# Kernel tuning notes

Hardware: AMD Instinct MI355X
Metric: run time of the kernel (lower is better)

Reference implementation:

```python
import jax, jax.numpy as jnp
import numpy as np

B, C, H, W = 16, 384, 56, 56
NH, WS, SS = 12, 7, 3          # num_heads, window_size, shift_size
MLP = 4 * C
N = WS * WS                     # tokens per window (49)
nHW = H // WS                   # windows per side (8)
nW = nHW * nHW                  # windows per image (64)
HD = C // NH                    # head dim (32)
EPS = 1e-5


def _ln(x, g, b):
    mu = jnp.mean(x, axis=-1, keepdims=True)
    var = jnp.mean(jnp.square(x - mu), axis=-1, keepdims=True)
    return (x - mu) * jax.lax.rsqrt(var + EPS) * g + b


def _attn_mask():
    # static shifted-window mask, computed once with numpy (constants)
    img = np.zeros((H, W))
    sl = (slice(0, -WS), slice(-WS, -SS), slice(-SS, None))
    cnt = 0
    for hs in sl:
        for ws_ in sl:
            img[hs, ws_] = cnt
            cnt += 1
    mw = img.reshape(nHW, WS, nHW, WS).transpose(0, 2, 1, 3).reshape(-1, N)
    d = mw[:, None, :] - mw[:, :, None]          # (nW, N, N)
    return jnp.asarray(np.where(d != 0, -100.0, 0.0), jnp.float32)

_MASK = _attn_mask()


def setup_inputs() -> dict:
    key = jax.random.key(0)
    ks = jax.random.split(key, 6)
    rn = lambda k, s: jax.random.normal(k, s, jnp.float32) * 0.02
    return {
        "x": jax.random.normal(ks[0], (B, C, H, W), jnp.float32),
        "norm1_g": jnp.ones((C,), jnp.float32),
        "norm1_b": jnp.zeros((C,), jnp.float32),
        "qkv_w": rn(ks[1], (C, 3 * C)),
        "qkv_b": jnp.zeros((3 * C,), jnp.float32),
        "proj_w": rn(ks[2], (C, C)),
        "proj_b": jnp.zeros((C,), jnp.float32),
        "norm2_g": jnp.ones((C,), jnp.float32),
        "norm2_b": jnp.zeros((C,), jnp.float32),
        "fc1_w": rn(ks[3], (C, MLP)),
        "fc1_b": jnp.zeros((MLP,), jnp.float32),
        "fc2_w": rn(ks[4], (MLP, C)),
        "fc2_b": jnp.zeros((C,), jnp.float32),
    }


def reference(x, norm1_g, norm1_b, qkv_w, qkv_b, proj_w, proj_b,
              norm2_g, norm2_b, fc1_w, fc1_b, fc2_w, fc2_b):
    shortcut = x                                   # (B, C, H, W)
    xh = jnp.transpose(x, (0, 2, 3, 1))            # (B, H, W, C)
    xh = _ln(xh, norm1_g, norm1_b)
    # H, W divisible by WS -> padding is a no-op; shifted window path
    xs = jnp.roll(xh, (-SS, -SS), axis=(1, 2))
    # window partition -> (B*nW, N, C)
    xw = xs.reshape(B, nHW, WS, nHW, WS, C).transpose(0, 1, 3, 2, 4, 5)
    xw = xw.reshape(-1, N, C)
    # attention
    qkv = (xw @ qkv_w + qkv_b).reshape(-1, N, 3, NH, HD).transpose(2, 0, 3, 1, 4)
    q, k, v = qkv[0] * HD ** -0.5, qkv[1], qkv[2]  # (B*nW, NH, N, HD)
    attn = jnp.einsum('whnd,whmd->whnm', q, k)     # (B*nW, NH, N, N)
    attn = attn.reshape(B, nW, NH, N, N) + _MASK[None, :, None]
    attn = jax.nn.softmax(attn, axis=-1).reshape(-1, NH, N, N)
    out = jnp.einsum('whnm,whmd->whnd', attn, v)   # (B*nW, NH, N, HD)
    out = out.transpose(0, 2, 1, 3).reshape(-1, N, C)
    out = out @ proj_w + proj_b
    # window reverse -> (B, H, W, C), un-shift
    xs = out.reshape(B, nHW, nHW, WS, WS, C).transpose(0, 1, 3, 2, 4, 5)
    xs = xs.reshape(B, H, W, C)
    xh = jnp.roll(xs, (SS, SS), axis=(1, 2))
    x2 = shortcut + jnp.transpose(xh, (0, 3, 1, 2))
    # MLP residual (in BHWC)
    xh2 = jnp.transpose(x2, (0, 2, 3, 1))
    h = jax.nn.gelu(_ln(xh2, norm2_g, norm2_b) @ fc1_w + fc1_b,
                    approximate=False) @ fc2_w + fc2_b
    xh2 = xh2 + h
    return jnp.transpose(xh2, (0, 3, 1, 2))
```

## Files before the change

### kernel.cpp

```cpp
#include <hip/hip_runtime.h>
#include <hip/hip_bf16.h>
#include <math.h>
#include <stdint.h>

#define C_ 384
#define TOKENS 50176

typedef __bf16 bf16;
typedef __bf16 bf16x8 __attribute__((ext_vector_type(8)));
typedef __bf16 bf16x4 __attribute__((ext_vector_type(4)));
typedef float  f32x4  __attribute__((ext_vector_type(4)));

__device__ __forceinline__ float b2f(bf16 x) { return (float)x; }
__device__ __forceinline__ bf16  f2b(float x) { return (bf16)x; }

__device__ __forceinline__ float fast_gelu(float v) {
    float u2 = v * fmaf(v * v, 0.07135481f, 1.5957691f);
    return v / (1.0f + __expf(-u2));
}

__device__ __forceinline__ void gld_lds16(const bf16* g, bf16* l) {
    __builtin_amdgcn_global_load_lds(
        (const __attribute__((address_space(1))) void*)g,
        (__attribute__((address_space(3))) void*)l, 16, 0, 0);
}

__global__ void wtrans_kernel(const float* __restrict__ in, bf16* __restrict__ out,
                              int K, int N) {
    int idx = blockIdx.x * 256 + threadIdx.x;
    if (idx >= K * N) return;
    int n = idx / K, k = idx % K;
    out[idx] = f2b(in[(size_t)k * N + n]);
}

__global__ __launch_bounds__(256) void ln1_gather_kernel(
    const float* __restrict__ x, const float* __restrict__ g,
    const float* __restrict__ bt, bf16* __restrict__ xw) {
    int wave = threadIdx.x >> 6, lane = threadIdx.x & 63;
    int T = blockIdx.x * 4 + wave;
    int wi = T / 49, n = T % 49;
    int b = wi >> 6, w64 = wi & 63;
    int bh = w64 >> 3, bw = w64 & 7;
    int hs = bh * 7 + n / 7 + 3; if (hs >= 56) hs -= 56;
    int wsd = bw * 7 + n % 7 + 3; if (wsd >= 56) wsd -= 56;
    const float* xp = x + (size_t)b * C_ * 3136 + hs * 56 + wsd;
    float v[6];
    #pragma unroll
    for (int k = 0; k < 6; k++) v[k] = xp[(size_t)(lane + k * 64) * 3136];
    float s = v[0] + v[1] + v[2] + v[3] + v[4] + v[5];
    #pragma unroll
    for (int m = 32; m; m >>= 1) s += __shfl_xor(s, m);
    float mu = s * (1.0f / 384.0f);
    float s2 = 0.f;
    #pragma unroll
    for (int k = 0; k < 6; k++) { float d = v[k] - mu; s2 += d * d; }
    #pragma unroll
    for (int m = 32; m; m >>= 1) s2 += __shfl_xor(s2, m);
    float rstd = rsqrtf(s2 * (1.0f / 384.0f) + 1e-5f);
    bf16* op = xw + (size_t)T * 384;
    #pragma unroll
    for (int k = 0; k < 6; k++) {
        int c = lane + k * 64;
        op[c] = f2b((v[k] - mu) * rstd * g[c] + bt[c]);
    }
}

enum { EPI_NONE = 0, EPI_GELU = 1, EPI_PROJ = 2, EPI_FC2 = 3 };

template <int EPI>
__global__ __launch_bounds__(256) void gemm_kernel(
    const bf16* __restrict__ A, const bf16* __restrict__ Wt,
    const float* __restrict__ bias, bf16* __restrict__ Cout,
    int Kdim, int Ndim,
    const float* __restrict__ resx,
    const bf16* __restrict__ resb) {
    __shared__ __align__(16) bf16 As[128 * 64];
    __shared__ __align__(16) bf16 Bs[128 * 64];
    int t = threadIdx.x;
    int m0 = blockIdx.x * 128, n0 = blockIdx.y * 128;
    int lane = t & 63, wave = t >> 6;
    int wr = wave >> 1, wc = wave & 1;
    int quad = lane >> 4, lm = lane & 15;
    f32x4 acc[4][4] = {};

    const bf16* gA[4]; const bf16* gB[4];
    bf16 *lA[4], *lB[4];
    #pragma unroll
    for (int p = 0; p < 4; p++) {
        int c = p * 256 + t;
        int row = c >> 3, g = c & 7;
        int gs = g ^ (row & 7);
        gA[p] = A  + (size_t)(m0 + row) * Kdim + gs * 8;
        gB[p] = Wt + (size_t)(n0 + row) * Kdim + gs * 8;
        lA[p] = As + c * 8;
        lB[p] = Bs + c * 8;
    }

    for (int k0 = 0; k0 < Kdim; k0 += 64) {
        #pragma unroll
        for (int p = 0; p < 4; p++) {
            gld_lds16(gA[p] + k0, lA[p]);
            gld_lds16(gB[p] + k0, lB[p]);
        }
        __syncthreads();
        #pragma unroll
        for (int kk = 0; kk < 2; kk++) {
            bf16x8 af[4], bfr[4];
            int grp = (kk * 4 + quad) ^ (lm & 7);
            #pragma unroll
            for (int i = 0; i < 4; i++)
                af[i] = *(const bf16x8*)(As + (wr * 64 + i * 16 + lm) * 64 + grp * 8);
            #pragma unroll
            for (int j = 0; j < 4; j++)
                bfr[j] = *(const bf16x8*)(Bs + (wc * 64 + j * 16 + lm) * 64 + grp * 8);
            #pragma unroll
            for (int j = 0; j < 4; j++)
                #pragma unroll
                for (int i = 0; i < 4; i++)
                    acc[j][i] = __builtin_amdgcn_mfma_f32_16x16x32_bf16(bfr[j], af[i], acc[j][i], 0, 0, 0);
        }
        __syncthreads();
    }

    #pragma unroll
    for (int i = 0; i < 4; i++) {
        int m = m0 + wr * 64 + i * 16 + lm;
        size_t resbase = 0;
        if (EPI == EPI_PROJ) {
            int wi = m / 49, n_ = m % 49;
            int b = wi >> 6, w64 = wi & 63;
            int bh = w64 >> 3, bw = w64 & 7;
            int hs = bh * 7 + n_ / 7 + 3; if (hs >= 56) hs -= 56;
            int wsd = bw * 7 + n_ % 7 + 3; if (wsd >= 56) wsd -= 56;
            resbase = (size_t)b * C_ * 3136 + hs * 56 + wsd;
        }
        #pragma unroll
        for (int j = 0; j < 4; j++) {
            int nb = n0 + wc * 64 + j * 16 + quad * 4;
            f32x4 bj = *(const f32x4*)(bias + nb);
            f32x4 v;
            #pragma unroll
            for (int r = 0; r < 4; r++) v[r] = acc[j][i][r] + bj[r];
            if (EPI == EPI_GELU) {
                #pragma unroll
                for (int r = 0; r < 4; r++) v[r] = fast_gelu(v[r]);
            }
            if (EPI == EPI_PROJ) {
                #pragma unroll
                for (int r = 0; r < 4; r++) v[r] += resx[resbase + (size_t)(nb + r) * 3136];
            }
            if (EPI == EPI_FC2) {
                bf16x4 rb = *(const bf16x4*)(resb + (size_t)m * 384 + nb);
                #pragma unroll
                for (int r = 0; r < 4; r++) v[r] += b2f(rb[r]);
            }
            bf16x4 o;
            #pragma unroll
            for (int r = 0; r < 4; r++) o[r] = f2b(v[r]);
            *(bf16x4*)(Cout + (size_t)m * Ndim + nb) = o;
        }
    }
}

__global__ __launch_bounds__(64) void attn_mfma_kernel(const bf16* __restrict__ qkv,
                                                       bf16* __restrict__ aout) {
    __shared__ __align__(16) bf16 pbuf[64 * 72];
    __shared__ int reg_[64];
    int l = threadIdx.x;
    int wi = blockIdx.x / 12, h = blockIdx.x % 12;
    int i16 = l & 15, quad = l >> 4;

    {
        int tok = l < 49 ? l : 48;
        int w64 = wi & 63;
        int bh = w64 >> 3, bw = w64 & 7;
        int hh = bh * 7 + tok / 7, ww = bw * 7 + tok % 7;
        int fh = hh < 49 ? 0 : (hh < 53 ? 1 : 2);
        int fw = ww < 49 ? 0 : (ww < 53 ? 1 : 2);
        reg_[l] = fh * 3 + fw;
    }
    __syncthreads();

    const bf16* qbase = qkv + (size_t)wi * 49 * 1152 + h * 32;

    f32x4 s_[4][4] = {};
    bf16x8 af[4], bfr[4];
    #pragma unroll
    for (int mi = 0; mi < 4; mi++) {
        int m = mi * 16 + i16; if (m > 48) m = 48;
        af[mi] = *(const bf16x8*)(qbase + (size_t)m * 1152 + quad * 8);
    }
    #pragma unroll
    for (int nt = 0; nt < 4; nt++) {
        int n = nt * 16 + i16; if (n > 48) n = 48;
        bfr[nt] = *(const bf16x8*)(qbase + 384 + (size_t)n * 1152 + quad * 8);
    }
    #pragma unroll
    for (int mi = 0; mi < 4; mi++)
        #pragma unroll
        for (int nt = 0; nt < 4; nt++)
            s_[mi][nt] = __builtin_amdgcn_mfma_f32_16x16x32_bf16(af[mi], bfr[nt], s_[mi][nt], 0, 0, 0);

    int creg[4];
    #pragma unroll
    for (int nt = 0; nt < 4; nt++) {
        int c = nt * 16 + i16; if (c > 48) c = 48;
        creg[nt] = reg_[c];
    }

    const float scale = 0.17677669529663687f;
    #pragma unroll
    for (int mi = 0; mi < 4; mi++) {
        #pragma unroll
        for (int r = 0; r < 4; r++) {
            int row = mi * 16 + quad * 4 + r;
            int rreg = reg_[row];
            float v[4]; float mx = -1e30f;
            #pragma unroll
            for (int nt = 0; nt < 4; nt++) {
                int c = nt * 16 + i16;
                float x = s_[mi][nt][r] * scale;
                if (c > 48) x = -1e30f;
                else if (rreg != creg[nt]) x -= 100.0f;
                v[nt] = x; mx = fmaxf(mx, x);
            }
            #pragma unroll
            for (int m = 8; m; m >>= 1) mx = fmaxf(mx, __shfl_xor(mx, m));
            float sum = 0.f;
            #pragma unroll
            for (int nt = 0; nt < 4; nt++) { v[nt] = __expf(v[nt] - mx); sum += v[nt]; }
            #pragma unroll
            for (int m = 8; m; m >>= 1) sum += __shfl_xor(sum, m);
            float inv = 1.0f / sum;
            #pragma unroll
            for (int nt = 0; nt < 4; nt++)
                pbuf[row * 72 + nt * 16 + i16] = f2b(v[nt] * inv);
        }
    }
    __syncthreads();

    f32x4 o_[4][2] = {};
    const bf16* vbase = qkv + (size_t)wi * 49 * 1152 + 768 + h * 32;
    #pragma unroll
    for (int ks = 0; ks < 2; ks++) {
        bf16x8 pa[4];
        #pragma unroll
        for (int mi = 0; mi < 4; mi++)
            pa[mi] = *(const bf16x8*)(pbuf + (mi * 16 + i16) * 72 + ks * 32 + quad * 8);
        bf16x8 vb[2];
        #pragma unroll
        for (int nt = 0; nt < 2; nt++)
            #pragma unroll
            for (int j = 0; j < 8; j++) {
                int tok = ks * 32 + quad * 8 + j; if (tok > 48) tok = 48;
                vb[nt][j] = vbase[(size_t)tok * 1152 + nt * 16 + i16];
            }
        #pragma unroll
        for (int mi = 0; mi < 4; mi++)
            #pragma unroll
            for (int nt = 0; nt < 2; nt++)
                o_[mi][nt] = __builtin_amdgcn_mfma_f32_16x16x32_bf16(pa[mi], vb[nt], o_[mi][nt], 0, 0, 0);
    }

    bf16* obase = aout + (size_t)wi * 49 * 384 + h * 32;
    #pragma unroll
    for (int mi = 0; mi < 4; mi++)
        #pragma unroll
        for (int r = 0; r < 4; r++) {
            int row = mi * 16 + quad * 4 + r;
            if (row < 49) {
                #pragma unroll
                for (int nt = 0; nt < 2; nt++)
                    obase[(size_t)row * 384 + nt * 16 + i16] = f2b(o_[mi][nt][r]);
            }
        }
}

__global__ __launch_bounds__(256) void ln2_kernel(const bf16* __restrict__ x2,
                                                  const float* __restrict__ g,
                                                  const float* __restrict__ bt,
                                                  bf16* __restrict__ x2n) {
    int wave = threadIdx.x >> 6, lane = threadIdx.x & 63;
    int T = blockIdx.x * 4 + wave;
    const bf16* xp = x2 + (size_t)T * 384;
    float v[6];
    #pragma unroll
    for (int k = 0; k < 6; k++) v[k] = b2f(xp[lane + k * 64]);
    float s = v[0] + v[1] + v[2] + v[3] + v[4] + v[5];
    #pragma unroll
    for (int m = 32; m; m >>= 1) s += __shfl_xor(s, m);
    float mu = s * (1.0f / 384.0f);
    float s2 = 0.f;
    #pragma unroll
    for (int k = 0; k < 6; k++) { float d = v[k] - mu; s2 += d * d; }
    #pragma unroll
    for (int m = 32; m; m >>= 1) s2 += __shfl_xor(s2, m);
    float rstd = rsqrtf(s2 * (1.0f / 384.0f) + 1e-5f);
    bf16* op = x2n + (size_t)T * 384;
    #pragma unroll
    for (int k = 0; k < 6; k++) {
        int c = lane + k * 64;
        op[c] = f2b((v[k] - mu) * rstd * g[c] + bt[c]);
    }
}

__global__ __launch_bounds__(256) void untile_kernel(const bf16* __restrict__ otok,
                                                     float* __restrict__ out) {
    __shared__ float tile[56 * 65];
    int t = threadIdx.x;
    int b = blockIdx.x / 336;
    int rem = blockIdx.x % 336;
    int h = rem / 6;
    int c0 = (rem % 6) * 64;
    int hs = h + 53; if (hs >= 56) hs -= 56;
    int bh = hs / 7, th = hs % 7;
    #pragma unroll
    for (int pass = 0; pass < 14; pass++) {
        int w = pass * 4 + (t >> 6);
        int c = t & 63;
        int wsd = w + 53; if (wsd >= 56) wsd -= 56;
        int T = (b * 64 + bh * 8 + wsd / 7) * 49 + th * 7 + wsd % 7;
        tile[w * 65 + c] = b2f(otok[(size_t)T * 384 + c0 + c]);
    }
    __syncthreads();
    #pragma unroll
    for (int pass = 0; pass < 14; pass++) {
        int idx = pass * 256 + t;
        int c = idx / 56, w = idx % 56;
        out[((size_t)(b * 384 + c0 + c)) * 3136 + h * 56 + w] = tile[w * 65 + c];
    }
}

extern "C" void kernel_launch(void* const* d_in, const int* in_sizes, int n_in,
                              void* d_out, int out_size, void* d_ws, size_t ws_size,
                              hipStream_t stream) {
    (void)in_sizes; (void)n_in; (void)out_size; (void)ws_size;
    const float* x      = (const float*)d_in[0];
    const float* n1g    = (const float*)d_in[1];
    const float* n1b    = (const float*)d_in[2];
    const float* qkv_w  = (const float*)d_in[3];
    const float* qkv_b  = (const float*)d_in[4];
    const float* proj_w = (const float*)d_in[5];
    const float* proj_b = (const float*)d_in[6];
    const float* n2g    = (const float*)d_in[7];
    const float* n2b    = (const float*)d_in[8];
    const float* fc1_w  = (const float*)d_in[9];
    const float* fc1_b  = (const float*)d_in[10];
    const float* fc2_w  = (const float*)d_in[11];
    const float* fc2_b  = (const float*)d_in[12];
    float* out = (float*)d_out;
    char* ws = (char*)d_ws;

    bf16* qkv_wT = (bf16*)(ws + 0);
    bf16* proj_wT = (bf16*)(ws + 884736);
    bf16* fc1_wT = (bf16*)(ws + 1179648);
    bf16* fc2_wT = (bf16*)(ws + 2359296);
    bf16* xw   = (bf16*)(ws + 4194304);
    bf16* qkvb = (bf16*)(ws + 42729472);
    bf16* attn = (bf16*)(ws + 158334976);
    bf16* x2   = (bf16*)(ws + 4194304);
    bf16* x2n  = (bf16*)(ws + 42729472);
    bf16* h1   = (bf16*)(ws + 81264640);
    bf16* otok = (bf16*)(ws + 235405312);

    wtrans_kernel<<<(384 * 1152 + 255) / 256, 256, 0, stream>>>(qkv_w, qkv_wT, 384, 1152);
    wtrans_kernel<<<(384 * 384 + 255) / 256, 256, 0, stream>>>(proj_w, proj_wT, 384, 384);
    wtrans_kernel<<<(384 * 1536 + 255) / 256, 256, 0, stream>>>(fc1_w, fc1_wT, 384, 1536);
    wtrans_kernel<<<(1536 * 384 + 255) / 256, 256, 0, stream>>>(fc2_w, fc2_wT, 1536, 384);

    ln1_gather_kernel<<<TOKENS / 4, 256, 0, stream>>>(x, n1g, n1b, xw);

    gemm_kernel<EPI_NONE><<<dim3(392, 9), 256, 0, stream>>>(
        xw, qkv_wT, qkv_b, qkvb, 384, 1152, nullptr, nullptr);

    attn_mfma_kernel<<<12288, 64, 0, stream>>>(qkvb, attn);

    gemm_kernel<EPI_PROJ><<<dim3(392, 3), 256, 0, stream>>>(
        attn, proj_wT, proj_b, x2, 384, 384, x, nullptr);

    ln2_kernel<<<TOKENS / 4, 256, 0, stream>>>(x2, n2g, n2b, x2n);

    gemm_kernel<EPI_GELU><<<dim3(392, 12), 256, 0, stream>>>(
        x2n, fc1_wT, fc1_b, h1, 384, 1536, nullptr, nullptr);

    gemm_kernel<EPI_FC2><<<dim3(392, 3), 256, 0, stream>>>(
        h1, fc2_wT, fc2_b, otok, 1536, 384, nullptr, x2);

    untile_kernel<<<16 * 336, 256, 0, stream>>>(otok, out);
}
```

Before: 736.2 us.

## Double-buffer GEMM LDS tiles with K=32 steps and XCD-aware block swizzle

The GEMM now uses two LDS buffers of K=32 each, issuing the next tile's global-to-LDS loads before computing on the current tile, with one barrier per iteration instead of two. This is meant to hide load latency behind the MFMA work. Block indices are also remapped so consecutive tiles land on the same XCD, and the grid is transposed so N-tiles vary fastest, which should improve L2 reuse of the A rows. The tradeoff is half as much MFMA work per barrier and a new swizzle pattern for the smaller tiles.

```diff
diff --git a/kernel.cpp b/kernel.cpp
--- a/kernel.cpp
+++ b/kernel.cpp
@@ -74,52 +74,65 @@
     int Kdim, int Ndim,
     const float* __restrict__ resx,
     const bf16* __restrict__ resb) {
-    __shared__ __align__(16) bf16 As[128 * 64];
-    __shared__ __align__(16) bf16 Bs[128 * 64];
+    __shared__ __align__(16) bf16 As[2][128 * 32];
+    __shared__ __align__(16) bf16 Bs[2][128 * 32];
     int t = threadIdx.x;
-    int m0 = blockIdx.x * 128, n0 = blockIdx.y * 128;
+
+    int nwg = gridDim.x * gridDim.y;
+    int bid = blockIdx.y * gridDim.x + blockIdx.x;
+    int q8 = nwg >> 3, r8 = nwg & 7, xcd = bid & 7, off = bid >> 3;
+    int swz = (xcd < r8 ? xcd * (q8 + 1) : r8 * (q8 + 1) + (xcd - r8) * q8) + off;
+    int n0 = (swz % gridDim.x) * 128;
+    int m0 = (swz / gridDim.x) * 128;
+
     int lane = t & 63, wave = t >> 6;
     int wr = wave >> 1, wc = wave & 1;
     int quad = lane >> 4, lm = lane & 15;
     f32x4 acc[4][4] = {};
 
-    const bf16* gA[4]; const bf16* gB[4];
-    bf16 *lA[4], *lB[4];
-    #pragma unroll
-    for (int p = 0; p < 4; p++) {
+    const bf16* gA[2]; const bf16* gB[2];
+    int lofs[2];
+    #pragma unroll
+    for (int p = 0; p < 2; p++) {
         int c = p * 256 + t;
-        int row = c >> 3, g = c & 7;
-        int gs = g ^ (row & 7);
+        int row = c >> 2, g = c & 3;
+        int gs = g ^ ((row >> 1) & 3);
         gA[p] = A  + (size_t)(m0 + row) * Kdim + gs * 8;
         gB[p] = Wt + (size_t)(n0 + row) * Kdim + gs * 8;
-        lA[p] = As + c * 8;
-        lB[p] = Bs + c * 8;
-    }
-
-    for (int k0 = 0; k0 < Kdim; k0 += 64) {
-        #pragma unroll
-        for (int p = 0; p < 4; p++) {
-            gld_lds16(gA[p] + k0, lA[p]);
-            gld_lds16(gB[p] + k0, lB[p]);
+        lofs[p] = c * 8;
+    }
+    int grp = quad ^ ((lm >> 1) & 3);
+
+    int nt = Kdim >> 5;
+    int cur = 0;
+    #pragma unroll
+    for (int p = 0; p < 2; p++) {
+        gld_lds16(gA[p], &As[0][lofs[p]]);
+        gld_lds16(gB[p], &Bs[0][lofs[p]]);
+    }
+    for (int tk = 0; tk < nt; ++tk) {
+        __syncthreads();
+        if (tk + 1 < nt) {
+            int k0 = (tk + 1) << 5;
+            #pragma unroll
+            for (int p = 0; p < 2; p++) {
+                gld_lds16(gA[p] + k0, &As[cur ^ 1][lofs[p]]);
+                gld_lds16(gB[p] + k0, &Bs[cur ^ 1][lofs[p]]);
+            }
         }
-        __syncthreads();
-        #pragma unroll
-        for (int kk = 0; kk < 2; kk++) {
-            bf16x8 af[4], bfr[4];
-            int grp = (kk * 4 + quad) ^ (lm & 7);
+        bf16x8 af[4], bfr[4];
+        #pragma unroll
+        for (int i = 0; i < 4; i++)
+            af[i] = *(const bf16x8*)(&As[cur][(wr * 64 + i * 16 + lm) * 32 + grp * 8]);
+        #pragma unroll
+        for (int j = 0; j < 4; j++)
+            bfr[j] = *(const bf16x8*)(&Bs[cur][(wc * 64 + j * 16 + lm) * 32 + grp * 8]);
+        #pragma unroll
+        for (int j = 0; j < 4; j++)
             #pragma unroll
             for (int i = 0; i < 4; i++)
-                af[i] = *(const bf16x8*)(As + (wr * 64 + i * 16 + lm) * 64 + grp * 8);
-            #pragma unroll
-            for (int j = 0; j < 4; j++)
-                bfr[j] = *(const bf16x8*)(Bs + (wc * 64 + j * 16 + lm) * 64 + grp * 8);
-            #pragma unroll
-            for (int j = 0; j < 4; j++)
-                #pragma unroll
-                for (int i = 0; i < 4; i++)
-                    acc[j][i] = __builtin_amdgcn_mfma_f32_16x16x32_bf16(bfr[j], af[i], acc[j][i], 0, 0, 0);
-        }
-        __syncthreads();
+                acc[j][i] = __builtin_amdgcn_mfma_f32_16x16x32_bf16(bfr[j], af[i], acc[j][i], 0, 0, 0);
+        cur ^= 1;
     }
 
     #pragma unroll
@@ -370,20 +383,20 @@
 
     ln1_gather_kernel<<<TOKENS / 4, 256, 0, stream>>>(x, n1g, n1b, xw);
 
-    gemm_kernel<EPI_NONE><<<dim3(392, 9), 256, 0, stream>>>(
+    gemm_kernel<EPI_NONE><<<dim3(9, 392), 256, 0, stream>>>(
         xw, qkv_wT, qkv_b, qkvb, 384, 1152, nullptr, nullptr);
 
     attn_mfma_kernel<<<12288, 64, 0, stream>>>(qkvb, attn);
 
-    gemm_kernel<EPI_PROJ><<<dim3(392, 3), 256, 0, stream>>>(
+    gemm_kernel<EPI_PROJ><<<dim3(3, 392), 256, 0, stream>>>(
         attn, proj_wT, proj_b, x2, 384, 384, x, nullptr);
 
     ln2_kernel<<<TOKENS / 4, 256, 0, stream>>>(x2, n2g, n2b, x2n);
 
-    gemm_kernel<EPI_GELU><<<dim3(392, 12), 256, 0, stream>>>(
+    gemm_kernel<EPI_GELU><<<dim3(12, 392), 256, 0, stream>>>(
         x2n, fc1_wT, fc1_b, h1, 384, 1536, nullptr, nullptr);
 
-    gemm_kernel<EPI_FC2><<<dim3(392, 3), 256, 0, stream>>>(
+    gemm_kernel<EPI_FC2><<<dim3(3, 392), 256, 0, stream>>>(
         h1, fc2_wT, fc2_b, otok, 1536, 384, nullptr, x2);
 
     untile_kernel<<<16 * 336, 256, 0, stream>>>(otok, out);
```

Result: faster. 715.8 us (-2.8%).

## Double-buffer GEMM LDS tiles with 256x128 blocks and XCD-aware block swizzle

Applied to the files above, without the earlier changes.

Restructures the bf16 GEMM to use 512-thread blocks computing 256x128 tiles, with two LDS buffers so global-to-LDS loads of the next K tile overlap MFMA work on the current one, using explicit vmcnt waits and barriers. It also remaps block IDs so consecutive tiles land on the same XCD for better L2 reuse of A and weight tiles, and raises MFMA priority with s_setprio. The larger LDS footprint (96 KB) and more threads per block may limit occupancy, and the manual waitcnt/barrier schedule is fragile.

```diff
diff --git a/kernel.cpp b/kernel.cpp
--- a/kernel.cpp
+++ b/kernel.cpp
@@ -67,59 +67,116 @@
 
 enum { EPI_NONE = 0, EPI_GELU = 1, EPI_PROJ = 2, EPI_FC2 = 3 };
 
+__device__ __forceinline__ void stage_tile(const bf16* const (&gA)[4], bf16* const (&lA)[4],
+                                           const bf16* const (&gB)[2], bf16* const (&lB)[2],
+                                           int k0) {
+    #pragma unroll
+    for (int p = 0; p < 4; p++) gld_lds16(gA[p] + k0, lA[p]);
+    #pragma unroll
+    for (int p = 0; p < 2; p++) gld_lds16(gB[p] + k0, lB[p]);
+}
+
+__device__ __forceinline__ void compute_tile(const bf16* Asb, const bf16* Bsb,
+                                             int wr, int wc, int quad, int lm,
+                                             f32x4 (&acc)[4][4]) {
+    #pragma unroll
+    for (int kk = 0; kk < 2; kk++) {
+        bf16x8 af[4], bfr[4];
+        #pragma unroll
+        for (int i = 0; i < 4; i++) {
+            int row = wr * 64 + i * 16 + lm;
+            int g = (kk * 4 + quad) ^ (row & 7);
+            af[i] = *(const bf16x8*)(Asb + row * 64 + g * 8);
+        }
+        #pragma unroll
+        for (int j = 0; j < 4; j++) {
+            int row = wc * 64 + j * 16 + lm;
+            int g = (kk * 4 + quad) ^ (row & 7);
+            bfr[j] = *(const bf16x8*)(Bsb + row * 64 + g * 8);
+        }
+        __builtin_amdgcn_s_setprio(1);
+        #pragma unroll
+        for (int j = 0; j < 4; j++)
+            #pragma unroll
+            for (int i = 0; i < 4; i++)
+                acc[j][i] = __builtin_amdgcn_mfma_f32_16x16x32_bf16(bfr[j], af[i], acc[j][i], 0, 0, 0);
+        __builtin_amdgcn_s_setprio(0);
+    }
+}
+
+#define SYNC_FENCE() do { __builtin_amdgcn_sched_barrier(0); \
+                          __builtin_amdgcn_s_barrier(); \
+                          __builtin_amdgcn_sched_barrier(0); } while (0)
+
 template <int EPI>
-__global__ __launch_bounds__(256) void gemm_kernel(
+__global__ __launch_bounds__(512, 2) void gemm_kernel(
     const bf16* __restrict__ A, const bf16* __restrict__ Wt,
     const float* __restrict__ bias, bf16* __restrict__ Cout,
     int Kdim, int Ndim,
     const float* __restrict__ resx,
     const bf16* __restrict__ resb) {
-    __shared__ __align__(16) bf16 As[128 * 64];
-    __shared__ __align__(16) bf16 Bs[128 * 64];
+    __shared__ __align__(16) bf16 As[2][256 * 64];
+    __shared__ __align__(16) bf16 Bs[2][128 * 64];
     int t = threadIdx.x;
-    int m0 = blockIdx.x * 128, n0 = blockIdx.y * 128;
+
+    int nwg = gridDim.x * gridDim.y;
+    int bid = blockIdx.y * gridDim.x + blockIdx.x;
+    int q8 = nwg >> 3, r8 = nwg & 7, xcd = bid & 7, off = bid >> 3;
+    int swz = (xcd < r8 ? xcd * (q8 + 1) : r8 * (q8 + 1) + (xcd - r8) * q8) + off;
+    int n0 = (swz % gridDim.x) * 128;
+    int m0 = (swz / gridDim.x) * 256;
+
     int lane = t & 63, wave = t >> 6;
     int wr = wave >> 1, wc = wave & 1;
     int quad = lane >> 4, lm = lane & 15;
     f32x4 acc[4][4] = {};
 
-    const bf16* gA[4]; const bf16* gB[4];
-    bf16 *lA[4], *lB[4];
+    const bf16* gA[4]; bf16* lA0[4]; bf16* lA1[4];
+    const bf16* gB[2]; bf16* lB0[2]; bf16* lB1[2];
     #pragma unroll
     for (int p = 0; p < 4; p++) {
-        int c = p * 256 + t;
-        int row = c >> 3, g = c & 7;
+        int idx = p * 512 + t;
+        int row = idx >> 3, g = idx & 7;
         int gs = g ^ (row & 7);
-        gA[p] = A  + (size_t)(m0 + row) * Kdim + gs * 8;
+        gA[p] = A + (size_t)(m0 + row) * Kdim + gs * 8;
+        lA0[p] = &As[0][idx * 8]; lA1[p] = &As[1][idx * 8];
+    }
+    #pragma unroll
+    for (int p = 0; p < 2; p++) {
+        int idx = p * 512 + t;
+        int row = idx >> 3, g = idx & 7;
+        int gs = g ^ (row & 7);
         gB[p] = Wt + (size_t)(n0 + row) * Kdim + gs * 8;
-        lA[p] = As + c * 8;
-        lB[p] = Bs + c * 8;
-    }
-
-    for (int k0 = 0; k0 < Kdim; k0 += 64) {
-        #pragma unroll
-        for (int p = 0; p < 4; p++) {
-            gld_lds16(gA[p] + k0, lA[p]);
-            gld_lds16(gB[p] + k0, lB[p]);
-        }
-        __syncthreads();
-        #pragma unroll
-        for (int kk = 0; kk < 2; kk++) {
-            bf16x8 af[4], bfr[4];
-            int grp = (kk * 4 + quad) ^ (lm & 7);
-            #pragma unroll
-            for (int i = 0; i < 4; i++)
-                af[i] = *(const bf16x8*)(As + (wr * 64 + i * 16 + lm) * 64 + grp * 8);
-            #pragma unroll
-            for (int j = 0; j < 4; j++)
-                bfr[j] = *(const bf16x8*)(Bs + (wc * 64 + j * 16 + lm) * 64 + grp * 8);
-            #pragma unroll
-            for (int j = 0; j < 4; j++)
-                #pragma unroll
-                for (int i = 0; i < 4; i++)
-                    acc[j][i] = __builtin_amdgcn_mfma_f32_16x16x32_bf16(bfr[j], af[i], acc[j][i], 0, 0, 0);
-        }
-        __syncthreads();
+        lB0[p] = &Bs[0][idx * 8]; lB1[p] = &Bs[1][idx * 8];
+    }
+
+    int nt = Kdim >> 6;
+    stage_tile(gA, lA0, gB, lB0, 0);
+    stage_tile(gA, lA1, gB, lB1, 64);
+    asm volatile("s_waitcnt vmcnt(6)" ::: "memory");
+    SYNC_FENCE();
+
+    for (int tk = 0; tk < nt; tk += 2) {
+        compute_tile(As[0], Bs[0], wr, wc, quad, lm, acc);
+        SYNC_FENCE();
+        if (tk + 2 < nt) {
+            stage_tile(gA, lA0, gB, lB0, (tk + 2) << 6);
+            asm volatile("s_waitcnt vmcnt(6)" ::: "memory");
+        } else {
+            asm volatile("s_waitcnt vmcnt(0)" ::: "memory");
+        }
+        SYNC_FENCE();
+        compute_tile(As[1], Bs[1], wr, wc, quad, lm, acc);
+        if (tk + 2 < nt) {
+            SYNC_FENCE();
+            if (tk + 3 < nt) {
+                stage_tile(gA, lA1, gB, lB1, (tk + 3) << 6);
+                asm volatile("s_waitcnt vmcnt(6)" ::: "memory");
+            } else {
+                asm volatile("s_waitcnt vmcnt(0)" ::: "memory");
+            }
+            SYNC_FENCE();
+        }
     }
 
     #pragma unroll
@@ -370,20 +427,20 @@
 
     ln1_gather_kernel<<<TOKENS / 4, 256, 0, stream>>>(x, n1g, n1b, xw);
 
-    gemm_kernel<EPI_NONE><<<dim3(392, 9), 256, 0, stream>>>(
+    gemm_kernel<EPI_NONE><<<dim3(9, 196), 512, 0, stream>>>(
         xw, qkv_wT, qkv_b, qkvb, 384, 1152, nullptr, nullptr);
 
     attn_mfma_kernel<<<12288, 64, 0, stream>>>(qkvb, attn);
 
-    gemm_kernel<EPI_PROJ><<<dim3(392, 3), 256, 0, stream>>>(
+    gemm_kernel<EPI_PROJ><<<dim3(3, 196), 512, 0, stream>>>(
         attn, proj_wT, proj_b, x2, 384, 384, x, nullptr);
 
     ln2_kernel<<<TOKENS / 4, 256, 0, stream>>>(x2, n2g, n2b, x2n);
 
-    gemm_kernel<EPI_GELU><<<dim3(392, 12), 256, 0, stream>>>(
+    gemm_kernel<EPI_GELU><<<dim3(12, 196), 512, 0, stream>>>(
         x2n, fc1_wT, fc1_b, h1, 384, 1536, nullptr, nullptr);
 
-    gemm_kernel<EPI_FC2><<<dim3(392, 3), 256, 0, stream>>>(
+    gemm_kernel<EPI_FC2><<<dim3(3, 196), 512, 0, stream>>>(
         h1, fc2_wT, fc2_b, otok, 1536, 384, nullptr, x2);
 
     untile_kernel<<<16 * 336, 256, 0, stream>>>(otok, out);
```

After: 701.7 us. 1.05x faster.
